# Optimization experiments

Measured on AMD Instinct MI355X. Metric: run time of the kernel, lower is better.

The kernel has to match this reference:

```python
import jax, jax.numpy as jnp
import numpy as np

EMBED_DIM = 1024
NUM_HEADS = 16
HEAD_DIM = EMBED_DIM // NUM_HEADS


def setup_inputs() -> dict:
    key = jax.random.key(0)
    ks = jax.random.split(key, 5)
    s = 1.0 / np.sqrt(EMBED_DIM)
    x = jax.random.normal(ks[0], (2, 2048, EMBED_DIM), dtype=jnp.float32)
    wq = jax.random.normal(ks[1], (EMBED_DIM, EMBED_DIM), dtype=jnp.float32) * s
    wk = jax.random.normal(ks[2], (EMBED_DIM, EMBED_DIM), dtype=jnp.float32) * s
    wv = jax.random.normal(ks[3], (EMBED_DIM, EMBED_DIM), dtype=jnp.float32) * s
    wo = jax.random.normal(ks[4], (EMBED_DIM, EMBED_DIM), dtype=jnp.float32) * s
    z = jnp.zeros((EMBED_DIM,), dtype=jnp.float32)
    return {"x": x, "wq": wq, "bq": z, "wk": wk, "bk": z, "wv": wv, "bv": z, "wo": wo, "bo": z}


def reference(x, wq, bq, wk, bk, wv, bv, wo, bo):
    B, S, D = x.shape
    H, Hd = NUM_HEADS, HEAD_DIM
    # projections -> [B, H, S, Hd]
    def proj(w, b):
        return (x @ w + b).reshape(B, S, H, Hd).transpose(0, 2, 1, 3)
    q = proj(wq, bq)
    k = proj(wk, bk)
    v = proj(wv, bv)
    scores = jnp.einsum('bhsd,bhtd->bhst', q, k) / jnp.sqrt(jnp.float32(Hd))
    probs = jax.nn.softmax(scores, axis=-1)
    attn = jnp.einsum('bhst,bhtd->bhsd', probs, v)  # [B,H,S,Hd]
    attn = attn.transpose(0, 2, 1, 3).reshape(B, S, D)
    return attn @ wo + bo
```

## Files before the change

### kernel.cpp

```cpp
#include <hip/hip_runtime.h>
#include <cstdint>

typedef __bf16 bf16_t;
typedef __bf16 bf16x4 __attribute__((ext_vector_type(4)));
typedef __bf16 bf16x8 __attribute__((ext_vector_type(8)));
typedef float floatx4 __attribute__((ext_vector_type(4)));

#define EMBED 1024
#define NHEAD 16
#define HDIM  64
#define SEQ   2048
#define BATCH 2
#define MTOT  (BATCH*SEQ)
#define QSCALE 0.18033688011112042f

__device__ __forceinline__ void gload16(const bf16_t* g, bf16_t* l) {
    __builtin_amdgcn_global_load_lds(
        (const __attribute__((address_space(1))) void*)g,
        (__attribute__((address_space(3))) void*)l, 16, 0, 0);
}

__global__ __launch_bounds__(256) void transpose4(
    const float* __restrict__ w0, const float* __restrict__ w1,
    const float* __restrict__ w2, const float* __restrict__ w3,
    const float* __restrict__ xin,
    bf16_t* __restrict__ out, bf16_t* __restrict__ xout)
{
    int z = blockIdx.z;
    int tx = threadIdx.x, ty = threadIdx.y;
    if (z >= 4) {
        const float* src = xin  + (size_t)(z - 4) * 1048576u;
        bf16_t*      dst = xout + (size_t)(z - 4) * 1048576u;
        int col = blockIdx.x * 32 + tx, rowb = blockIdx.y * 32;
#pragma unroll
        for (int j = 0; j < 4; j++) {
            int rr = rowb + ty + 8 * j;
            dst[(size_t)rr * 1024 + col] = (bf16_t)src[(size_t)rr * 1024 + col];
        }
        return;
    }
    __shared__ float t[32][33];
    const float* src = (z == 0) ? w0 : (z == 1) ? w1 : (z == 2) ? w2 : w3;
    bf16_t* dst = out + (size_t)z * 1048576u;
    int bx = blockIdx.x * 32, by = blockIdx.y * 32;
#pragma unroll
    for (int j = 0; j < 4; j++)
        t[ty + 8 * j][tx] = src[(size_t)(by + ty + 8 * j) * EMBED + bx + tx];
    __syncthreads();
#pragma unroll
    for (int j = 0; j < 4; j++)
        dst[(size_t)(bx + ty + 8 * j) * EMBED + by + tx] = (bf16_t)t[tx][ty + 8 * j];
}

template<int BM, int MODE>
__global__ __launch_bounds__(256) void gemm_t(
    const bf16_t* __restrict__ A,  const bf16_t* __restrict__ Bt,
    const float* __restrict__ bias0, const float* __restrict__ bias1,
    const float* __restrict__ bias2,
    void* __restrict__ outraw, bf16_t* __restrict__ vtout,
    int M, int N, int K)
{
    constexpr int MS = BM / 32;
    constexpr int NA = BM / 32;
    __shared__ __align__(16) bf16_t smem[BM * 64 + 128 * 64];
    bf16_t (*As)[64] = (bf16_t(*)[64])smem;
    bf16_t (*Bs)[64] = (bf16_t(*)[64])(smem + BM * 64);

    int tid  = threadIdx.x;
    int m0   = blockIdx.y * BM, n0 = blockIdx.x * 128;
    int wv   = tid >> 6, lane = tid & 63;
    int wr   = wv >> 1,  wc   = wv & 1;
    int quad = lane >> 4, l16 = lane & 15;
    int lr   = lane >> 3, lq = lane & 7;
    int sw   = (l16 & 7) * 8;
    int wch  = (lq ^ lr) * 8;

    floatx4 acc[MS][4];
    floatx4 z4 = {0.f, 0.f, 0.f, 0.f};
#pragma unroll
    for (int mi = 0; mi < MS; mi++)
#pragma unroll
        for (int ni = 0; ni < 4; ni++) acc[mi][ni] = z4;

    bf16x8 sa[NA], sb[4];
    auto LOADG = [&](int k0) {
#pragma unroll
        for (int i = 0; i < NA; i++)
            sa[i] = *(const bf16x8*)
                &A[(size_t)(m0 + wv * (BM / 4) + i * 8 + lr) * K + k0 + lq * 8];
#pragma unroll
        for (int i = 0; i < 4; i++)
            sb[i] = *(const bf16x8*)
                &Bt[(size_t)(n0 + wv * 32 + i * 8 + lr) * K + k0 + lq * 8];
    };
    auto STOREG = [&]() {
#pragma unroll
        for (int i = 0; i < NA; i++)
            *(bf16x8*)&As[wv * (BM / 4) + i * 8 + lr][wch] = sa[i];
#pragma unroll
        for (int i = 0; i < 4; i++)
            *(bf16x8*)&Bs[wv * 32 + i * 8 + lr][wch] = sb[i];
    };

    LOADG(0);
    for (int k0 = 0; k0 < K; k0 += 64) {
        STOREG();
        __syncthreads();
        if (k0 + 64 < K) LOADG(k0 + 64);
#pragma unroll
        for (int kk = 0; kk < 2; kk++) {
            bf16x8 af[MS], bfr[4];
            int co = kk * 32 + quad * 8;
#pragma unroll
            for (int i = 0; i < MS; i++)
                af[i]  = *(const bf16x8*)&As[wr * (BM / 2) + i * 16 + l16][co ^ sw];
#pragma unroll
            for (int i = 0; i < 4; i++)
                bfr[i] = *(const bf16x8*)&Bs[wc * 64 + i * 16 + l16][co ^ sw];
#pragma unroll
            for (int mi = 0; mi < MS; mi++)
#pragma unroll
                for (int ni = 0; ni < 4; ni++)
                    acc[mi][ni] = __builtin_amdgcn_mfma_f32_16x16x32_bf16(
                        af[mi], bfr[ni], acc[mi][ni], 0, 0, 0);
        }
        if (k0 + 64 < K) __syncthreads();
    }

    if constexpr (MODE == 1) {
        if (n0 >= 2048) {
            bf16_t (*Ts)[72] = (bf16_t(*)[72])smem;
            int bb = m0 >> 11, s0 = m0 & 2047;
            int hd0 = n0 & 1023;
#pragma unroll
            for (int mh = 0; mh < 2; mh++) {
                __syncthreads();
                if (wr == mh) {
#pragma unroll
                    for (int mi = 0; mi < MS; mi++)
#pragma unroll
                        for (int ni = 0; ni < 4; ni++)
#pragma unroll
                            for (int r = 0; r < 4; r++) {
                                int ml = mi * 16 + quad * 4 + r;
                                int nl = wc * 64 + ni * 16 + l16;
                                float v = acc[mi][ni][r] + bias2[hd0 + nl];
                                int sp = ((ml >> 5) << 5) | (((ml >> 2) & 3) << 3)
                                       | (((ml >> 4) & 1) << 2) | (ml & 3);
                                Ts[nl][sp] = (bf16_t)v;
                            }
                }
                __syncthreads();
#pragma unroll
                for (int i = 0; i < 4; i++) {
                    int c = tid + i * 256;
                    int row = c >> 3, ch = (c & 7) * 8;
                    int hh = row >> 6, dd = row & 63;
                    size_t off = (((size_t)bb * NHEAD + (hd0 >> 6) + hh) * HDIM + dd) * SEQ
                               + (size_t)(s0 + mh * 64 + ch);
                    *(bf16x8*)&vtout[off] = *(const bf16x8*)&Ts[row][ch];
                }
            }
            return;
        }
    }

#pragma unroll
    for (int mi = 0; mi < MS; mi++) {
#pragma unroll
        for (int ni = 0; ni < 4; ni++) {
            int n = n0 + wc * 64 + ni * 16 + l16;
#pragma unroll
            for (int r = 0; r < 4; r++) {
                int m = m0 + wr * (BM / 2) + mi * 16 + quad * 4 + r;
                float v = acc[mi][ni][r];
                if (MODE == 0) {
                    ((float*)outraw)[(size_t)m * N + n] = v + bias0[n];
                } else {
                    int which = n >> 10, cc = n & 1023;
                    v += (which == 0) ? bias0[cc] : bias1[cc];
                    if (which == 0) v *= QSCALE;
                    int h = cc >> 6, d = cc & 63;
                    int b = m >> 11, s = m & 2047;
                    ((bf16_t*)outraw)[(size_t)which * 4194304u +
                        (((size_t)b * NHEAD + h) * SEQ + s) * HDIM + d] = (bf16_t)v;
                }
            }
        }
    }
}

__global__ __launch_bounds__(256) void attn_mfma(
    const bf16_t* __restrict__ Q, const bf16_t* __restrict__ K,
    const bf16_t* __restrict__ Vt, bf16_t* __restrict__ O)
{
    __shared__ __align__(16) bf16_t Ks[2][64][64];
    __shared__ __align__(16) bf16_t Vs[2][64][64];

    int tid  = threadIdx.x;
    int wv   = tid >> 6, lane = tid & 63;
    int quad = lane >> 4, l16 = lane & 15;
    int lr   = lane >> 3, lq = lane & 7;
    int sw   = (l16 & 7) * 8;
    int flat = blockIdx.x;
    int hb   = flat & 31;
    int qt   = flat >> 5;
    int h = hb & 15, b = hb >> 4;
    int bh = b * NHEAD + h;
    int qw = qt * 128 + wv * 32;

    const bf16_t* Qb = Q  + (size_t)bh * SEQ * HDIM;
    const bf16_t* Kb = K  + (size_t)bh * SEQ * HDIM;
    const bf16_t* Vb = Vt + (size_t)bh * SEQ * HDIM;

    const bf16_t* kg = Kb + (size_t)(wv * 16 + lr) * HDIM + (lq ^ lr) * 8;
    const bf16_t* vg = Vb + (size_t)(wv * 16 + lr) * SEQ  + (lq ^ lr) * 8;

    bf16x8 qf[2][2];
#pragma unroll
    for (int ms = 0; ms < 2; ms++)
#pragma unroll
        for (int kk = 0; kk < 2; kk++)
            qf[ms][kk] = *(const bf16x8*)
                &Qb[(size_t)(qw + ms * 16 + l16) * HDIM + kk * 32 + quad * 8];

    floatx4 o_acc[2][4];
    floatx4 z4  = {0.f, 0.f, 0.f, 0.f};
    floatx4 m16 = {-16.f, -16.f, -16.f, -16.f};
#pragma unroll
    for (int ms = 0; ms < 2; ms++)
#pragma unroll
        for (int nd = 0; nd < 4; nd++) o_acc[ms][nd] = z4;
    float l_i[2] = {0.f, 0.f};

    gload16(kg,           &Ks[0][wv * 16][0]);
    gload16(kg + 512,     &Ks[0][wv * 16 + 8][0]);
    gload16(vg,           &Vs[0][wv * 16][0]);
    gload16(vg + 8 * SEQ, &Vs[0][wv * 16 + 8][0]);

    for (int t = 0; t < 32; t++) {
        int cur = t & 1;
        __syncthreads();
        if (t < 31) {
            const bf16_t* kn = kg + (size_t)(t + 1) * 4096;
            const bf16_t* vn = vg + (size_t)(t + 1) * 64;
            int nb = cur ^ 1;
            gload16(kn,           &Ks[nb][wv * 16][0]);
            gload16(kn + 512,     &Ks[nb][wv * 16 + 8][0]);
            gload16(vn,           &Vs[nb][wv * 16][0]);
            gload16(vn + 8 * SEQ, &Vs[nb][wv * 16 + 8][0]);
        }

        floatx4 st[2][4];
#pragma unroll
        for (int ms = 0; ms < 2; ms++)
#pragma unroll
            for (int ns = 0; ns < 4; ns++) st[ms][ns] = m16;
#pragma unroll
        for (int ns = 0; ns < 4; ns++) {
#pragma unroll
            for (int kk = 0; kk < 2; kk++) {
                bf16x8 kf = *(const bf16x8*)
                    &Ks[cur][ns * 16 + l16][(kk * 32 + quad * 8) ^ sw];
#pragma unroll
                for (int ms = 0; ms < 2; ms++)
                    st[ms][ns] = __builtin_amdgcn_mfma_f32_16x16x32_bf16(
                        kf, qf[ms][kk], st[ms][ns], 0, 0, 0);
            }
        }

        bf16x8 pf[2][2];
#pragma unroll
        for (int ms = 0; ms < 2; ms++) {
            float ls = 0.f;
#pragma unroll
            for (int kk = 0; kk < 2; kk++)
#pragma unroll
                for (int tt = 0; tt < 8; tt++) {
                    float p = __builtin_amdgcn_exp2f(st[ms][2 * kk + (tt >> 2)][tt & 3]);
                    ls += p;
                    pf[ms][kk][tt] = (bf16_t)p;
                }
            l_i[ms] += ls;
        }

#pragma unroll
        for (int nd = 0; nd < 4; nd++) {
#pragma unroll
            for (int kk = 0; kk < 2; kk++) {
                bf16x8 vf = *(const bf16x8*)
                    &Vs[cur][nd * 16 + l16][(kk * 32 + quad * 8) ^ sw];
#pragma unroll
                for (int ms = 0; ms < 2; ms++)
                    o_acc[ms][nd] = __builtin_amdgcn_mfma_f32_16x16x32_bf16(
                        vf, pf[ms][kk], o_acc[ms][nd], 0, 0, 0);
            }
        }
    }

#pragma unroll
    for (int ms = 0; ms < 2; ms++) {
        float l = l_i[ms];
        l += __shfl_xor(l, 16);
        l += __shfl_xor(l, 32);
        float inv = 1.f / l;
        int q = qw + ms * 16 + l16;
        bf16_t* ob = O + ((size_t)b * SEQ + q) * EMBED + h * HDIM;
#pragma unroll
        for (int nd = 0; nd < 4; nd++)
#pragma unroll
            for (int r = 0; r < 4; r++)
                ob[nd * 16 + quad * 4 + r] = (bf16_t)(o_acc[ms][nd][r] * inv);
    }
}

extern "C" void kernel_launch(void* const* d_in, const int* in_sizes, int n_in,
                              void* d_out, int out_size, void* d_ws, size_t ws_size,
                              hipStream_t stream)
{
    const float* x  = (const float*)d_in[0];
    const float* wq = (const float*)d_in[1];
    const float* bq = (const float*)d_in[2];
    const float* wk = (const float*)d_in[3];
    const float* bk = (const float*)d_in[4];
    const float* wv = (const float*)d_in[5];
    const float* bv = (const float*)d_in[6];
    const float* wo = (const float*)d_in[7];
    const float* bo = (const float*)d_in[8];

    char*   ws    = (char*)d_ws;
    bf16_t* Wt    = (bf16_t*)ws;
    bf16_t* Xb    = (bf16_t*)(ws + 8ull  * 1024 * 1024);
    bf16_t* QKV   = (bf16_t*)(ws + 16ull * 1024 * 1024);
    bf16_t* Vt    = (bf16_t*)(ws + 40ull * 1024 * 1024);
    bf16_t* attnO = (bf16_t*)(ws + 48ull * 1024 * 1024);
    float*  outp  = (float*)d_out;

    transpose4<<<dim3(32, 32, 8), dim3(32, 8), 0, stream>>>(
        wq, wk, wv, wo, x, Wt, Xb);

    gemm_t<128, 1><<<dim3(24, 32), 256, 0, stream>>>(
        Xb, Wt, bq, bk, bv, QKV, Vt, MTOT, 3072, EMBED);

    attn_mfma<<<dim3(512), 256, 0, stream>>>(
        QKV, QKV + 4194304u, Vt, attnO);

    gemm_t<64, 0><<<dim3(8, 64), 256, 0, stream>>>(
        attnO, Wt + 3u * 1048576u, bo, bo, bo, outp, nullptr, MTOT, EMBED, EMBED);
}
```

Measured before the change: 193.3 us.

## Double-buffer GEMM tiles with direct global-to-LDS loads and remap block order

Replaces the register-staged global→LDS copy in the projection GEMMs with `global_load_lds` DMA into a double-buffered shared-memory tile. The next K-tile is fetched while the current one is consumed, and one barrier per iteration is dropped. Blocks are also launched on a 1D grid with a remapped tile order, so consecutive block IDs share B columns across groups of 8 M-tiles for better cache locality. This doubles LDS per block, which may lower occupancy, and it relies on correct waitcnt handling for the async LDS loads.

```diff
diff --git a/kernel.cpp b/kernel.cpp
--- a/kernel.cpp
+++ b/kernel.cpp
@@ -61,19 +61,21 @@
     int M, int N, int K)
 {
     constexpr int MS = BM / 32;
-    constexpr int NA = BM / 32;
-    __shared__ __align__(16) bf16_t smem[BM * 64 + 128 * 64];
-    bf16_t (*As)[64] = (bf16_t(*)[64])smem;
-    bf16_t (*Bs)[64] = (bf16_t(*)[64])(smem + BM * 64);
+    constexpr int BUFSZ = (BM + 128) * 64;
+    __shared__ __align__(16) bf16_t smem[2 * BUFSZ];
 
     int tid  = threadIdx.x;
-    int m0   = blockIdx.y * BM, n0 = blockIdx.x * 128;
+    int id   = blockIdx.x;
+    int c8   = id & 7, rr_ = id >> 3;
+    int nblk = N >> 7;
+    int n0   = (rr_ % nblk) * 128;
+    int m0   = ((rr_ / nblk) * 8 + c8) * BM;
     int wv   = tid >> 6, lane = tid & 63;
     int wr   = wv >> 1,  wc   = wv & 1;
     int quad = lane >> 4, l16 = lane & 15;
     int lr   = lane >> 3, lq = lane & 7;
     int sw   = (l16 & 7) * 8;
-    int wch  = (lq ^ lr) * 8;
+    int lcs  = ((lq ^ lr) * 8);
 
     floatx4 acc[MS][4];
     floatx4 z4 = {0.f, 0.f, 0.f, 0.f};
@@ -82,31 +84,29 @@
 #pragma unroll
         for (int ni = 0; ni < 4; ni++) acc[mi][ni] = z4;
 
-    bf16x8 sa[NA], sb[4];
-    auto LOADG = [&](int k0) {
-#pragma unroll
-        for (int i = 0; i < NA; i++)
-            sa[i] = *(const bf16x8*)
-                &A[(size_t)(m0 + wv * (BM / 4) + i * 8 + lr) * K + k0 + lq * 8];
-#pragma unroll
-        for (int i = 0; i < 4; i++)
-            sb[i] = *(const bf16x8*)
-                &Bt[(size_t)(n0 + wv * 32 + i * 8 + lr) * K + k0 + lq * 8];
+    auto STAGE = [&](int k0, int buf) {
+        bf16_t* as = smem + buf * BUFSZ;
+        bf16_t* bs = as + BM * 64;
+#pragma unroll
+        for (int i = 0; i < BM / 32; i++) {
+            int r = wv * (BM / 4) + i * 8;
+            gload16(&A[(size_t)(m0 + r + lr) * K + k0 + lcs], as + r * 64);
+        }
+#pragma unroll
+        for (int i = 0; i < 4; i++) {
+            int r = wv * 32 + i * 8;
+            gload16(&Bt[(size_t)(n0 + r + lr) * K + k0 + lcs], bs + r * 64);
+        }
     };
-    auto STOREG = [&]() {
-#pragma unroll
-        for (int i = 0; i < NA; i++)
-            *(bf16x8*)&As[wv * (BM / 4) + i * 8 + lr][wch] = sa[i];
-#pragma unroll
-        for (int i = 0; i < 4; i++)
-            *(bf16x8*)&Bs[wv * 32 + i * 8 + lr][wch] = sb[i];
-    };
-
-    LOADG(0);
-    for (int k0 = 0; k0 < K; k0 += 64) {
-        STOREG();
+
+    STAGE(0, 0);
+    int T = K >> 6;
+    for (int t = 0; t < T; t++) {
+        int cur = t & 1;
         __syncthreads();
-        if (k0 + 64 < K) LOADG(k0 + 64);
+        if (t + 1 < T) STAGE((t + 1) << 6, cur ^ 1);
+        bf16_t (*As)[64] = (bf16_t(*)[64])(smem + cur * BUFSZ);
+        bf16_t (*Bs)[64] = (bf16_t(*)[64])(smem + cur * BUFSZ + BM * 64);
 #pragma unroll
         for (int kk = 0; kk < 2; kk++) {
             bf16x8 af[MS], bfr[4];
@@ -124,7 +124,6 @@
                     acc[mi][ni] = __builtin_amdgcn_mfma_f32_16x16x32_bf16(
                         af[mi], bfr[ni], acc[mi][ni], 0, 0, 0);
         }
-        if (k0 + 64 < K) __syncthreads();
     }
 
     if constexpr (MODE == 1) {
@@ -339,12 +338,12 @@
     transpose4<<<dim3(32, 32, 8), dim3(32, 8), 0, stream>>>(
         wq, wk, wv, wo, x, Wt, Xb);
 
-    gemm_t<128, 1><<<dim3(24, 32), 256, 0, stream>>>(
+    gemm_t<128, 1><<<dim3(768), 256, 0, stream>>>(
         Xb, Wt, bq, bk, bv, QKV, Vt, MTOT, 3072, EMBED);
 
     attn_mfma<<<dim3(512), 256, 0, stream>>>(
         QKV, QKV + 4194304u, Vt, attnO);
 
-    gemm_t<64, 0><<<dim3(8, 64), 256, 0, stream>>>(
+    gemm_t<64, 0><<<dim3(512), 256, 0, stream>>>(
         attnO, Wt + 3u * 1048576u, bo, bo, bo, outp, nullptr, MTOT, EMBED, EMBED);
 }
```

After: 180.8 us. -6.4%, faster.
